# Optimization experiments

Hardware: AMD Instinct MI355X
Metric: run time of the kernel (lower is better)

The kernel has to match this reference:

```python
import jax, jax.numpy as jnp
import numpy as np

XDIM = 3 * 2 * 14 * 14  # 1176, asserted in original temporal_pool
KM_ITERS = 10           # k-means iterations
TEMPORAL_LEN = 120 // 2  # self.temporal_length
SPATIAL_LEN = 60 // 2    # self.spatial_length


def temporal_pool(x, t, h, w):
    x = x.reshape(t, h // 2, w // 2, 2, 2, 3, 2, 14, 14)
    x = x.transpose(0, 1, 2, 5, 6, 3, 7, 4, 8)  # (t,h/2,w/2,3,2, 2,14, 2,14)
    x = x.reshape(-1, 6, 28, 28)
    # F.avg_pool2d(kernel=2, stride=2)
    x = x.reshape(-1, 6, 14, 2, 14, 2).mean(axis=(3, 5))
    x = x.reshape(t, h // 2, w // 2, 3, 2, 14, 14)
    nh, nw = (h // 2) // 2, (w // 2) // 2
    x = x.reshape(t, nh, 2, nw, 2, 3, 2, 14, 14)
    x = x.transpose(0, 1, 3, 2, 4, 5, 6, 7, 8)
    x = x.reshape(t, nh, nw, 4 * XDIM).reshape(-1, XDIM)
    return x, (t, nh * 2, nw * 2)


def _sqdist(A, B):
    # squared euclidean distances, [M,D]x[N,D] -> [M,N]
    A2 = jnp.sum(A * A, axis=1, keepdims=True)
    B2 = jnp.sum(B * B, axis=1, keepdims=True)
    return A2 + B2.T - 2.0 * (A @ B.T)


def weighted_kmeans_ordered(xf, k):
    # xf: [t, Dv] per-frame flattened features; uniform frame weights
    t = xf.shape[0]
    init_idx = jnp.round(jnp.linspace(0.0, t - 1.0, k)).astype(jnp.int32)
    cent0 = xf[init_idx]

    def step(cent, _):
        assign = jnp.argmin(_sqdist(xf, cent), axis=1)      # [t]
        oh = jax.nn.one_hot(assign, k, dtype=xf.dtype)      # [t,k]
        counts = oh.sum(axis=0)                             # [k]
        new = (oh.T @ xf) / jnp.maximum(counts, 1.0)[:, None]
        cent = jnp.where(counts[:, None] > 0, new, cent)
        return cent, None

    cent, _ = jax.lax.scan(step, cent0, None, length=KM_ITERS)
    assign = jnp.argmin(_sqdist(xf, cent), axis=1)
    oh = jax.nn.one_hot(assign, k, dtype=xf.dtype)
    counts = oh.sum(axis=0)                                  # cluster weights
    times = (oh.T @ jnp.arange(t, dtype=xf.dtype)) / jnp.maximum(counts, 1.0)
    order = jnp.argsort(times)                               # 'ordered': sort by mean timestamp
    return cent[order], counts[order], jnp.round(times[order]).astype(jnp.int32)


def setup_inputs() -> dict:
    key = jax.random.key(0)
    t, h, w = 256, 16, 16
    x = jax.random.normal(key, (t * (h // 2) * (w // 2) * 4, XDIM), dtype=jnp.float32)
    return {"x": x, "t": t, "h": h, "w": w}


def reference(x, t, h, w):
    small_x, (_, sh, sw) = temporal_pool(x, t, h, w)      # sh=h//2, sw=w//2
    per_frame = (sh // 2) * (sw // 2) * 4                  # pooled tokens per frame
    xs = small_x.reshape(t, per_frame * XDIM)              # [t, Dv] per-frame vectors

    # 2) temporal compress (CSM memory): weighted k-means, clusters ordered by time
    cent, weights, timestamps = weighted_kmeans_ordered(xs, TEMPORAL_LEN)
    tem_x = cent.reshape(TEMPORAL_LEN * per_frame, XDIM)

    # 3) spatial enhance (DAM memory): k-largest clusters retrieve nearest frames (euclidean)
    order = jnp.argsort(-weights)
    klarge = order[:SPATIAL_LEN]
    centroids = cent[klarge]                               # [SPATIAL_LEN, Dv]
    dist = jnp.sqrt(jnp.maximum(_sqdist(centroids, xs), 0.0))
    idx = jnp.argmin(dist, axis=1)                         # retrieved frame indices
    x_frames = x.reshape(t, (h // 2) * (w // 2) * 4, XDIM)
    spa_x = x_frames[idx].reshape(-1, XDIM)

    # 4) concatenate spatial + temporal memories (grouped in 2x2 token blocks)
    cat_x = jnp.concatenate(
        [spa_x.reshape(-1, 4, XDIM), tem_x.reshape(-1, 4, XDIM)], axis=0
    ).reshape(-1, XDIM)
    return cat_x, idx, timestamps, weights
```

## Files before the change

kernel.cpp:

```cpp
#include <hip/hip_runtime.h>
#include <hip/hip_bf16.h>
#include <math.h>

#define GK 75264
#define NF 256
#define KC 60
#define NSEL 30
#define NCH 196
#define KM_IT 10

typedef __attribute__((ext_vector_type(8))) short bf16x8;
typedef __attribute__((ext_vector_type(4))) float f32x4;
typedef __attribute__((ext_vector_type(8))) unsigned short u16x8;

__device__ __forceinline__ float b2f(unsigned short u) {
  union { unsigned u32; float f; } c; c.u32 = ((unsigned)u) << 16; return c.f;
}

__global__ void pool_kernel(const float* __restrict__ x,
                            __hip_bfloat16* __restrict__ H,
                            __hip_bfloat16* __restrict__ M) {
  unsigned id = blockIdx.x * 256u + threadIdx.x;
  unsigned m = id / 1176u, o = id - m * 1176u;
  unsigned t = m >> 6, r = m & 63u;
  unsigned ih = r >> 4, iw = (r >> 2) & 3u, s = r & 3u;
  unsigned i8 = ih * 2u + (s >> 1), j8 = iw * 2u + (s & 1u);
  unsigned c = o / 392u, o2 = o - c * 392u;
  unsigned d = o2 / 196u, o3 = o2 - d * 196u;
  unsigned e = o3 / 14u, f = o3 - e * 14u;
  unsigned a = (e >= 7u) ? 1u : 0u, b = (f >= 7u) ? 1u : 0u;
  unsigned ee = 2u * e - 14u * a, ff = 2u * f - 14u * b;
  unsigned xrow = ((t * 8u + i8) * 8u + j8) * 4u + a * 2u + b;
  unsigned xcol = ((c * 2u + d) * 14u + ee) * 14u + ff;
  const float* base = x + (size_t)xrow * 1176u + xcol;
  float v = 0.25f * ((base[0] + base[1]) + (base[14] + base[15]));
  __hip_bfloat16 hb = __float2bfloat16(v);
  float hf = __bfloat162float(hb);
  __hip_bfloat16 mb = __float2bfloat16(v - hf);
  H[id] = hb;
  M[id] = mb;
}

__global__ __launch_bounds__(512) void gram_mfma(const unsigned short* __restrict__ HB,
                                                 const unsigned short* __restrict__ MB,
                                                 float* __restrict__ gpart) {
  __shared__ __align__(16) char sH[256 * 64];
  __shared__ __align__(16) char sM[256 * 64];
  const int ch = blockIdx.x;
  const int t = threadIdx.x;
  const int w = t >> 6, l = t & 63;
  const int rs = w >> 1, cs = w & 1;
  const int lg = l >> 4, lr = l & 15;

  f32x4 acc[4][8];
#pragma unroll
  for (int i = 0; i < 4; ++i)
#pragma unroll
    for (int j = 0; j < 8; ++j) acc[i][j] = (f32x4){0.f, 0.f, 0.f, 0.f};

  for (int step = 0; step < 12; ++step) {
    const int k0 = ch * 384 + step * 32;
#pragma unroll
    for (int cc = 0; cc < 2; ++cc) {
      int c = t + cc * 512;
      int row = c >> 2, kc = c & 3;
      size_t goff = (size_t)row * GK + k0 + kc * 8;
      u16x8 vh = *(const u16x8*)(HB + goff);
      u16x8 vm = *(const u16x8*)(MB + goff);
      int lo = row * 64 + ((kc * 16) ^ (((row >> 1) & 3) << 4));
      *(u16x8*)(sH + lo) = vh;
      *(u16x8*)(sM + lo) = vm;
    }
    __syncthreads();

    bf16x8 Ah[4], Am[4];
#pragma unroll
    for (int tr = 0; tr < 4; ++tr) {
      int row = rs * 64 + tr * 16 + lr;
      int off = row * 64 + ((lg * 16) ^ (((row >> 1) & 3) << 4));
      Ah[tr] = *(const bf16x8*)(sH + off);
      Am[tr] = *(const bf16x8*)(sM + off);
    }
#pragma unroll
    for (int tc = 0; tc < 8; ++tc) {
      int col = cs * 128 + tc * 16 + lr;
      int boff = col * 64 + ((lg * 16) ^ (((col >> 1) & 3) << 4));
      bf16x8 Bh = *(const bf16x8*)(sH + boff);
      bf16x8 Bm = *(const bf16x8*)(sM + boff);
#pragma unroll
      for (int tr = 0; tr < 4; ++tr) {
        acc[tr][tc] = __builtin_amdgcn_mfma_f32_16x16x32_bf16(Ah[tr], Bh, acc[tr][tc], 0, 0, 0);
        acc[tr][tc] = __builtin_amdgcn_mfma_f32_16x16x32_bf16(Ah[tr], Bm, acc[tr][tc], 0, 0, 0);
        acc[tr][tc] = __builtin_amdgcn_mfma_f32_16x16x32_bf16(Am[tr], Bh, acc[tr][tc], 0, 0, 0);
      }
    }
    __syncthreads();
  }

  float* outp = gpart + (size_t)ch * 65536;
#pragma unroll
  for (int tr = 0; tr < 4; ++tr)
#pragma unroll
    for (int tc = 0; tc < 8; ++tc) {
#pragma unroll
      for (int r = 0; r < 4; ++r) {
        int grow = rs * 64 + tr * 16 + lg * 4 + r;
        int gcol = cs * 128 + tc * 16 + lr;
        outp[grow * 256 + gcol] = acc[tr][tc][r];
      }
    }
}

__global__ void reduceG(const float* __restrict__ gpart, double* __restrict__ G) {
  int i = blockIdx.x, j = threadIdx.x;
  double s = 0.0;
  for (int c = 0; c < NCH; ++c) s += (double)gpart[(size_t)c * 65536 + i * 256 + j];
  G[i * 256 + j] = s;
}

__global__ __launch_bounds__(1024) void kmeans_all(
    const double* __restrict__ G,
    int* __restrict__ orderws, int* __restrict__ idxws,
    int* __restrict__ mcount, int* __restrict__ mlist, int* __restrict__ Nout,
    float* __restrict__ out_idx, float* __restrict__ out_ts, float* __restrict__ out_w) {
  __shared__ double S[KC][256];
  __shared__ double giiL[256];
  __shared__ double pminD[4][256];
  __shared__ int    pminJ[4][256];
  __shared__ __align__(16) double qi[KC][2];
  __shared__ int Ns[KC];
  __shared__ unsigned long long membw[KC][4];
  __shared__ unsigned long long membwN[KC][4];
  __shared__ int counts64[64], tsum64[64];
  __shared__ float times[KC], wts[KC];
  __shared__ int ord[KC], ord2[KC], sel[NSEL];

  const int tid = threadIdx.x;
  const int i = tid & 255;
  const int z = tid >> 8;
  const int lane = tid & 63;
  const int wv4 = (tid >> 6) & 3;
  const int wid = tid >> 6;

  if (tid < KC) {
    int pj = (int)rint((double)tid * 255.0 / 59.0);
    double q = G[(size_t)pj * 257];
    qi[tid][0] = q; qi[tid][1] = 1.0;
    Ns[tid] = 1;
  }
  if (tid < 256) giiL[tid] = G[(size_t)tid * 257];
  for (int j = wid; j < KC; j += 16) {
    int pj = (int)rint((double)j * 255.0 / 59.0);
    const double* row = G + (size_t)pj * 256 + lane;
    double c0 = row[0], c1 = row[64], c2 = row[128], c3 = row[192];
    S[j][lane] = c0; S[j][64 + lane] = c1; S[j][128 + lane] = c2; S[j][192 + lane] = c3;
  }
  if (z == 0) {
    for (int j = 0; j < KC; ++j) {
      int pj = (int)rint((double)j * 255.0 / 59.0);
      unsigned long long mm = __ballot(i == pj);
      if (lane == 0) membw[j][wv4] = mm;
    }
  }
  __syncthreads();

  const double gii = giiL[i];

  for (int it = 0; it < KM_IT; ++it) {
    {
      double bd = 1e300; int bj = 0;
#pragma unroll
      for (int t = 0; t < 15; ++t) {
        int j = z * 15 + t;
        double2 qv = *(const double2*)&qi[j][0];
        double dd = gii + qv.x - 2.0 * S[j][i] * qv.y;
        if (dd < bd) { bd = dd; bj = j; }
      }
      pminD[z][i] = bd; pminJ[z][i] = bj;
    }
    __syncthreads();

    if (z == 0) {
      double bd = pminD[0][i]; int bb = pminJ[0][i];
#pragma unroll
      for (int g = 1; g < 4; ++g) {
        double d2 = pminD[g][i];
        if (d2 < bd) { bd = d2; bb = pminJ[g][i]; }
      }
      for (int j = 0; j < KC; ++j) {
        unsigned long long mm = __ballot(bb == j);
        if (lane == 0) membwN[j][wv4] = mm;
      }
    }
    __syncthreads();

    for (int j = wid; j < KC; j += 16) {
      unsigned long long mw0 = membwN[j][0], mw1 = membwN[j][1];
      unsigned long long mw2 = membwN[j][2], mw3 = membwN[j][3];
      int c = __builtin_popcountll(mw0) + __builtin_popcountll(mw1)
            + __builtin_popcountll(mw2) + __builtin_popcountll(mw3);
      if (c == 0) continue;
      int d = (mw0 != membw[j][0]) | (mw1 != membw[j][1])
            | (mw2 != membw[j][2]) | (mw3 != membw[j][3]);
      if (!d) continue;
      if (lane == 0) {
        membw[j][0] = mw0; membw[j][1] = mw1; membw[j][2] = mw2; membw[j][3] = mw3;
      }
      double a0 = 0.0, a1 = 0.0, a2 = 0.0, a3 = 0.0;
#pragma unroll
      for (int w = 0; w < 4; ++w) {
        unsigned long long mm = membwN[j][w];
        const double* gb = G + (size_t)w * 64 * 256;
        while (mm) {
          int bs[4];
#pragma unroll
          for (int k = 0; k < 4; ++k) {
            if (mm) { bs[k] = __builtin_ctzll(mm); mm &= mm - 1; } else bs[k] = -1;
          }
          double g0[4], g1[4], g2[4], g3[4];
#pragma unroll
          for (int k = 0; k < 4; ++k) {
            if (bs[k] >= 0) {
              const double* row = gb + (size_t)bs[k] * 256 + lane;
              g0[k] = row[0]; g1[k] = row[64]; g2[k] = row[128]; g3[k] = row[192];
            } else { g0[k] = 0.0; g1[k] = 0.0; g2[k] = 0.0; g3[k] = 0.0; }
          }
#pragma unroll
          for (int k = 0; k < 4; ++k) {
            a0 += g0[k]; a1 += g1[k]; a2 += g2[k]; a3 += g3[k];
          }
        }
      }
      S[j][lane] = a0; S[j][64 + lane] = a1; S[j][128 + lane] = a2; S[j][192 + lane] = a3;

      double q = 0.0;
#define QFOLD_WORD(MASK, AREG)                                                \
      {                                                                       \
        unsigned long long mm = (MASK);                                       \
        while (mm) {                                                          \
          int b0 = -1, b1 = -1, b2 = -1, b3 = -1;                             \
          if (mm) { b0 = __builtin_ctzll(mm); mm &= mm - 1; }                 \
          if (mm) { b1 = __builtin_ctzll(mm); mm &= mm - 1; }                 \
          if (mm) { b2 = __builtin_ctzll(mm); mm &= mm - 1; }                 \
          if (mm) { b3 = __builtin_ctzll(mm); mm &= mm - 1; }                 \
          double s0 = (b0 >= 0) ? __shfl((AREG), b0, 64) : 0.0;               \
          double s1 = (b1 >= 0) ? __shfl((AREG), b1, 64) : 0.0;               \
          double s2 = (b2 >= 0) ? __shfl((AREG), b2, 64) : 0.0;               \
          double s3 = (b3 >= 0) ? __shfl((AREG), b3, 64) : 0.0;               \
          q += s0; q += s1; q += s2; q += s3;                                 \
        }                                                                     \
      }
      QFOLD_WORD(mw0, a0)
      QFOLD_WORD(mw1, a1)
      QFOLD_WORD(mw2, a2)
      QFOLD_WORD(mw3, a3)
#undef QFOLD_WORD
      if (lane == 0) {
        double n = (double)c;
        Ns[j] = c;
        qi[j][1] = 1.0 / n;
        qi[j][0] = q / (n * n);
      }
    }
    __syncthreads();
  }

  {
    double bd = 1e300; int bj = 0;
#pragma unroll
    for (int t = 0; t < 15; ++t) {
      int j = z * 15 + t;
      double2 qv = *(const double2*)&qi[j][0];
      double dd = gii + qv.x - 2.0 * S[j][i] * qv.y;
      if (dd < bd) { bd = dd; bj = j; }
    }
    pminD[z][i] = bd; pminJ[z][i] = bj;
  }
  if (tid < 64) { counts64[tid] = 0; tsum64[tid] = 0; }
  __syncthreads();
  if (z == 0) {
    double bd = pminD[0][i]; int bb = pminJ[0][i];
#pragma unroll
    for (int g = 1; g < 4; ++g) {
      double d2 = pminD[g][i];
      if (d2 < bd) { bd = d2; bb = pminJ[g][i]; }
    }
    atomicAdd(&counts64[bb], 1);
    atomicAdd(&tsum64[bb], i);
  }
  __syncthreads();
  if (tid < KC) times[tid] = (float)tsum64[tid] / fmaxf((float)counts64[tid], 1.0f);
  __syncthreads();
  if (tid < KC) {
    float ti = times[tid]; int r = 0;
    for (int s = 0; s < KC; ++s) {
      float ts = times[s];
      r += (ts < ti) || (ts == ti && s < tid);
    }
    ord[r] = tid;
  }
  __syncthreads();
  if (tid < KC) wts[tid] = (float)counts64[ord[tid]];
  __syncthreads();
  if (tid < KC) {
    float wi = wts[tid]; int r = 0;
    for (int s = 0; s < KC; ++s) {
      float wsv = wts[s];
      r += (wsv > wi) || (wsv == wi && s < tid);
    }
    ord2[r] = tid;
  }
  __syncthreads();
  if (tid < KC) {
    int j = ord[tid];
    orderws[tid] = j;
    out_w[tid] = (float)counts64[j];
    out_ts[tid] = rintf(times[j]);
    Nout[tid] = Ns[tid];
  }
  if (tid < NSEL) sel[tid] = ord[ord2[tid]];
  if (tid < KC) {
    int c = 0;
#pragma unroll
    for (int w = 0; w < 4; ++w) {
      unsigned long long mm = membw[tid][w];
      while (mm) {
        int b = __builtin_ctzll(mm);
        mlist[tid * 256 + (c++)] = w * 64 + b;
        mm &= mm - 1;
      }
    }
    mcount[tid] = c;
  }
  __syncthreads();

  {
    for (int s = wid; s < NSEL; s += 16) {
      int j = sel[s];
      double qn = qi[j][0], iv = qi[j][1];
      unsigned long long key = ~0ULL;
#pragma unroll
      for (int q = 0; q < 4; ++q) {
        int p = lane + 64 * q;
        double v = giiL[p] + qn - 2.0 * S[j][p] * iv;
        float dd = sqrtf(fmaxf((float)v, 0.0f));
        unsigned long long k = (((unsigned long long)__float_as_uint(dd)) << 32) | (unsigned)p;
        if (k < key) key = k;
      }
#pragma unroll
      for (int o = 32; o > 0; o >>= 1) {
        unsigned long long other = __shfl_xor(key, o, 64);
        if (other < key) key = other;
      }
      if (lane == 0) { int bi = (int)(key & 0xffffffffULL); idxws[s] = bi; out_idx[s] = (float)bi; }
    }
  }
}

__global__ void tail_kernel(const float* __restrict__ x, const int* __restrict__ idxws,
                            const __hip_bfloat16* __restrict__ HB,
                            const __hip_bfloat16* __restrict__ MB,
                            const int* __restrict__ orderws,
                            const int* __restrict__ mcount, const int* __restrict__ mlist,
                            const int* __restrict__ N,
                            float* __restrict__ out_cat, float* __restrict__ out_tem) {
  int bid = blockIdx.x;
  if (bid < 8820) {
    int pos = bid * 256 + threadIdx.x;
    int s = pos / 75264;
    int o = pos - s * 75264;
    ((float4*)out_cat)[pos] = ((const float4*)x)[(size_t)idxws[s] * 75264 + o];
  } else {
    int b2 = bid - 8820;
    int r = b2 / 37, g = b2 - r * 37;
    int col8 = g * 256 + threadIdx.x;
    if (col8 >= 9408) return;
    int j = orderws[r];
    int cntm = mcount[j];
    float n = (float)N[j];
    float acc[8];
#pragma unroll
    for (int k = 0; k < 8; ++k) acc[k] = 0.f;
    for (int m = 0; m < cntm; ++m) {
      int p = mlist[j * 256 + m];
      u16x8 hv = *(const u16x8*)((const unsigned short*)HB + (size_t)p * GK + (size_t)col8 * 8);
      u16x8 mv = *(const u16x8*)((const unsigned short*)MB + (size_t)p * GK + (size_t)col8 * 8);
#pragma unroll
      for (int k = 0; k < 8; ++k) acc[k] += b2f(hv[k]) + b2f(mv[k]);
    }
    float4 o0 = make_float4(acc[0] / n, acc[1] / n, acc[2] / n, acc[3] / n);
    float4 o1 = make_float4(acc[4] / n, acc[5] / n, acc[6] / n, acc[7] / n);
    float4* dst = (float4*)out_tem + (size_t)r * 18816 + (size_t)col8 * 2;
    dst[0] = o0;
    dst[1] = o1;
  }
}

extern "C" void kernel_launch(void* const* d_in, const int* in_sizes, int n_in,
                              void* d_out, int out_size, void* d_ws, size_t ws_size,
                              hipStream_t stream) {
  const float* x = (const float*)d_in[0];
  char* ws = (char*)d_ws;
  size_t off = 0;
  __hip_bfloat16* HB = (__hip_bfloat16*)(ws + off); off += (size_t)19267584 * 2;
  __hip_bfloat16* MB = (__hip_bfloat16*)(ws + off); off += (size_t)19267584 * 2;
  double* G    = (double*)(ws + off);    off += (size_t)65536 * 8;
  int* orderws = (int*)(ws + off);       off += 256;
  int* idxws   = (int*)(ws + off);       off += 256;
  int* mcount  = (int*)(ws + off);       off += 256;
  int* Nws     = (int*)(ws + off);       off += 256;
  int* mlist   = (int*)(ws + off);       off += (size_t)KC * 256 * 4;

  float* out = (float*)d_out;
  float* gpart = out;

  const size_t o_cat = 0;
  const size_t o_tem = 9031680;
  const size_t o_idx = 13547520;
  const size_t o_ts  = o_idx + 30;
  const size_t o_w   = o_ts + 60;

  pool_kernel<<<75264, 256, 0, stream>>>(x, HB, MB);
  gram_mfma<<<NCH, 512, 0, stream>>>((const unsigned short*)HB, (const unsigned short*)MB, gpart);
  reduceG<<<256, 256, 0, stream>>>(gpart, G);
  kmeans_all<<<1, 1024, 0, stream>>>(G, orderws, idxws, mcount, mlist, Nws,
                                     out + o_idx, out + o_ts, out + o_w);
  tail_kernel<<<8820 + KC * 37, 256, 0, stream>>>(x, idxws, HB, MB, orderws, mcount, mlist,
                                                  Nws, out + o_cat, out + o_tem);
}
```

Before: 222.9 us.

## Replicate argmin across thread groups, drop partial-min barrier, use xor-shuffle reduction

Each of the four 256-thread groups now computes the full 60-way argmin redundantly instead of splitting candidates and merging through shared memory. This removes one __syncthreads and the pminD/pminJ shared arrays per k-means iteration, and spreads the membership ballots across all 16 waves. The per-cluster squared-norm fold switches from serial ctz/shuffle loops to a masked per-lane sum followed by an xor-shuffle tree reduction. The cost is 4x redundant distance work per iteration, and the summation order changes in double precision.

```diff
diff --git a/kernel.cpp b/kernel.cpp
--- a/kernel.cpp
+++ b/kernel.cpp
@@ -125,8 +125,6 @@
     float* __restrict__ out_idx, float* __restrict__ out_ts, float* __restrict__ out_w) {
   __shared__ double S[KC][256];
   __shared__ double giiL[256];
-  __shared__ double pminD[4][256];
-  __shared__ int    pminJ[4][256];
   __shared__ __align__(16) double qi[KC][2];
   __shared__ int Ns[KC];
   __shared__ unsigned long long membw[KC][4];
@@ -139,8 +137,9 @@
   const int i = tid & 255;
   const int z = tid >> 8;
   const int lane = tid & 63;
-  const int wv4 = (tid >> 6) & 3;
   const int wid = tid >> 6;
+  const int wb = wid & 3;
+  const int wa = wid >> 2;
 
   if (tid < KC) {
     int pj = (int)rint((double)tid * 255.0 / 59.0);
@@ -155,42 +154,29 @@
     double c0 = row[0], c1 = row[64], c2 = row[128], c3 = row[192];
     S[j][lane] = c0; S[j][64 + lane] = c1; S[j][128 + lane] = c2; S[j][192 + lane] = c3;
   }
-  if (z == 0) {
+#pragma unroll
+  for (int t = 0; t < 15; ++t) {
+    int j = wa + 4 * t;
+    int pj = (int)rint((double)j * 255.0 / 59.0);
+    unsigned long long mm = __ballot(i == pj);
+    if (lane == 0) membw[j][wb] = mm;
+  }
+  __syncthreads();
+
+  const double gii = giiL[i];
+
+  for (int it = 0; it < KM_IT; ++it) {
+    double bd = 1e300; int bb = 0;
     for (int j = 0; j < KC; ++j) {
-      int pj = (int)rint((double)j * 255.0 / 59.0);
-      unsigned long long mm = __ballot(i == pj);
-      if (lane == 0) membw[j][wv4] = mm;
-    }
-  }
-  __syncthreads();
-
-  const double gii = giiL[i];
-
-  for (int it = 0; it < KM_IT; ++it) {
-    {
-      double bd = 1e300; int bj = 0;
-#pragma unroll
-      for (int t = 0; t < 15; ++t) {
-        int j = z * 15 + t;
-        double2 qv = *(const double2*)&qi[j][0];
-        double dd = gii + qv.x - 2.0 * S[j][i] * qv.y;
-        if (dd < bd) { bd = dd; bj = j; }
-      }
-      pminD[z][i] = bd; pminJ[z][i] = bj;
-    }
-    __syncthreads();
-
-    if (z == 0) {
-      double bd = pminD[0][i]; int bb = pminJ[0][i];
-#pragma unroll
-      for (int g = 1; g < 4; ++g) {
-        double d2 = pminD[g][i];
-        if (d2 < bd) { bd = d2; bb = pminJ[g][i]; }
-      }
-      for (int j = 0; j < KC; ++j) {
-        unsigned long long mm = __ballot(bb == j);
-        if (lane == 0) membwN[j][wv4] = mm;
-      }
+      double2 qv = *(const double2*)&qi[j][0];
+      double dd = gii + qv.x - 2.0 * S[j][i] * qv.y;
+      if (dd < bd) { bd = dd; bb = j; }
+    }
+#pragma unroll
+    for (int t = 0; t < 15; ++t) {
+      int j = wa + 4 * t;
+      unsigned long long mm = __ballot(bb == j);
+      if (lane == 0) membwN[j][wb] = mm;
     }
     __syncthreads();
 
@@ -233,57 +219,31 @@
       }
       S[j][lane] = a0; S[j][64 + lane] = a1; S[j][128 + lane] = a2; S[j][192 + lane] = a3;
 
-      double q = 0.0;
-#define QFOLD_WORD(MASK, AREG)                                                \
-      {                                                                       \
-        unsigned long long mm = (MASK);                                       \
-        while (mm) {                                                          \
-          int b0 = -1, b1 = -1, b2 = -1, b3 = -1;                             \
-          if (mm) { b0 = __builtin_ctzll(mm); mm &= mm - 1; }                 \
-          if (mm) { b1 = __builtin_ctzll(mm); mm &= mm - 1; }                 \
-          if (mm) { b2 = __builtin_ctzll(mm); mm &= mm - 1; }                 \
-          if (mm) { b3 = __builtin_ctzll(mm); mm &= mm - 1; }                 \
-          double s0 = (b0 >= 0) ? __shfl((AREG), b0, 64) : 0.0;               \
-          double s1 = (b1 >= 0) ? __shfl((AREG), b1, 64) : 0.0;               \
-          double s2 = (b2 >= 0) ? __shfl((AREG), b2, 64) : 0.0;               \
-          double s3 = (b3 >= 0) ? __shfl((AREG), b3, 64) : 0.0;               \
-          q += s0; q += s1; q += s2; q += s3;                                 \
-        }                                                                     \
-      }
-      QFOLD_WORD(mw0, a0)
-      QFOLD_WORD(mw1, a1)
-      QFOLD_WORD(mw2, a2)
-      QFOLD_WORD(mw3, a3)
-#undef QFOLD_WORD
+      double ql = 0.0;
+      ql += ((mw0 >> lane) & 1ULL) ? a0 : 0.0;
+      ql += ((mw1 >> lane) & 1ULL) ? a1 : 0.0;
+      ql += ((mw2 >> lane) & 1ULL) ? a2 : 0.0;
+      ql += ((mw3 >> lane) & 1ULL) ? a3 : 0.0;
+#pragma unroll
+      for (int o = 32; o > 0; o >>= 1) ql += __shfl_xor(ql, o, 64);
       if (lane == 0) {
         double n = (double)c;
         Ns[j] = c;
         qi[j][1] = 1.0 / n;
-        qi[j][0] = q / (n * n);
+        qi[j][0] = ql / (n * n);
       }
     }
     __syncthreads();
   }
 
-  {
-    double bd = 1e300; int bj = 0;
-#pragma unroll
-    for (int t = 0; t < 15; ++t) {
-      int j = z * 15 + t;
+  if (tid < 64) { counts64[tid] = 0; tsum64[tid] = 0; }
+  __syncthreads();
+  if (z == 0) {
+    double bd = 1e300; int bb = 0;
+    for (int j = 0; j < KC; ++j) {
       double2 qv = *(const double2*)&qi[j][0];
       double dd = gii + qv.x - 2.0 * S[j][i] * qv.y;
-      if (dd < bd) { bd = dd; bj = j; }
-    }
-    pminD[z][i] = bd; pminJ[z][i] = bj;
-  }
-  if (tid < 64) { counts64[tid] = 0; tsum64[tid] = 0; }
-  __syncthreads();
-  if (z == 0) {
-    double bd = pminD[0][i]; int bb = pminJ[0][i];
-#pragma unroll
-    for (int g = 1; g < 4; ++g) {
-      double d2 = pminD[g][i];
-      if (d2 < bd) { bd = d2; bb = pminJ[g][i]; }
+      if (dd < bd) { bd = dd; bb = j; }
     }
     atomicAdd(&counts64[bb], 1);
     atomicAdd(&tsum64[bb], i);
```

After: 233.0 us. 4.5% more time.
